# Optimization experiments

Hardware: AMD Instinct MI355X
Metric: run time of the kernel (lower is better)

Reference implementation:

```python
import jax, jax.numpy as jnp
import numpy as np

EMBED_DIM = 2048
NUM_Q_HEADS = 16
NUM_KV_HEADS = 4
HEAD_DIM = EMBED_DIM // NUM_Q_HEADS  # 128
N_REP = NUM_Q_HEADS // NUM_KV_HEADS  # 4


def setup_inputs() -> dict:
    key = jax.random.key(0)
    ks = jax.random.split(key, 8)
    B, T, C = 2, 2048, EMBED_DIM
    s = 0.02
    return {
        "x": jax.random.normal(ks[0], (B, T, C), dtype=jnp.float32),
        "Wq": jax.random.normal(ks[1], (C, NUM_Q_HEADS * HEAD_DIM), dtype=jnp.float32) * s,
        "bq": jax.random.normal(ks[2], (NUM_Q_HEADS * HEAD_DIM,), dtype=jnp.float32) * s,
        "Wk": jax.random.normal(ks[3], (C, NUM_KV_HEADS * HEAD_DIM), dtype=jnp.float32) * s,
        "bk": jax.random.normal(ks[4], (NUM_KV_HEADS * HEAD_DIM,), dtype=jnp.float32) * s,
        "Wv": jax.random.normal(ks[5], (C, NUM_KV_HEADS * HEAD_DIM), dtype=jnp.float32) * s,
        "bv": jax.random.normal(ks[6], (NUM_KV_HEADS * HEAD_DIM,), dtype=jnp.float32) * s,
        "Wo": jax.random.normal(ks[7], (C, C), dtype=jnp.float32) * s,
    }


def reference(x, Wq, bq, Wk, bk, Wv, bv, Wo):
    B, T, C = x.shape
    # Projections (torch Linear with bias; weights stored as [in, out])
    q = (x @ Wq + bq).reshape(B, T, NUM_KV_HEADS, N_REP, HEAD_DIM)
    k = (x @ Wk + bk).reshape(B, T, NUM_KV_HEADS, HEAD_DIM)
    v = (x @ Wv + bv).reshape(B, T, NUM_KV_HEADS, HEAD_DIM)
    # GQA: group query heads per kv head instead of materializing repeated K/V.
    # q: [B, G, n_rep, Tq, d], k/v: [B, G, Tk, d]
    q = q.transpose(0, 2, 3, 1, 4)  # B, G, n_rep, T, d
    k = k.transpose(0, 2, 1, 3)     # B, G, T, d
    v = v.transpose(0, 2, 1, 3)
    scale = 1.0 / jnp.sqrt(jnp.asarray(HEAD_DIM, dtype=x.dtype))
    scores = jnp.einsum('bgnqd,bgkd->bgnqk', q, k) * scale
    attn = jax.nn.softmax(scores, axis=-1)
    out = jnp.einsum('bgnqk,bgkd->bgnqd', attn, v)  # B, G, n_rep, T, d
    # merge heads back: (G, n_rep) -> Hq, then [B, T, C]
    out = out.transpose(0, 3, 1, 2, 4).reshape(B, T, C)
    return out @ Wo
```

## Files before the change

kernel.cpp:

```cpp
#include <hip/hip_runtime.h>
#include <hip/hip_bf16.h>
#include <cstdint>
#include <cstddef>

typedef __bf16 bf16;
typedef __attribute__((ext_vector_type(8))) __bf16 bf16x8;
typedef __attribute__((ext_vector_type(4))) float f32x4;
typedef __attribute__((ext_vector_type(16))) float f32x16;

#define KPAD 136
#define VPAD 72

__device__ __forceinline__ void async16(const void* g, void* l) {
  __builtin_amdgcn_global_load_lds(
      (const __attribute__((address_space(1))) void*)g,
      (__attribute__((address_space(3))) void*)l,
      16, 0, 0);
}

__global__ void cvt_x(const float* __restrict__ in, bf16* __restrict__ out, int n8) {
  int i = blockIdx.x * 256 + threadIdx.x;
  if (i >= n8) return;
  const float* src = in + (size_t)i * 8;
  float4 f0 = *reinterpret_cast<const float4*>(src);
  float4 f1 = *reinterpret_cast<const float4*>(src + 4);
  bf16x8 v = {(bf16)f0.x, (bf16)f0.y, (bf16)f0.z, (bf16)f0.w,
              (bf16)f1.x, (bf16)f1.y, (bf16)f1.z, (bf16)f1.w};
  *reinterpret_cast<bf16x8*>(out + (size_t)i * 8) = v;
}

template <typename CT, bool HAS_BIAS>
__global__ __launch_bounds__(256, 2)
void gemm_bt(const bf16* __restrict__ A, const bf16* __restrict__ Bt,
             const bf16* __restrict__ bias, CT* __restrict__ C,
             int M, int N, int K) {
  __shared__ bf16 smem[4][128 * 64];
  const int tid = threadIdx.x;
  const int wave = tid >> 6, lane = tid & 63;
  const int quad = lane >> 4, l15 = lane & 15;
  const int row0 = blockIdx.y * 128;
  const int col0 = blockIdx.x * 128;
  const int wm = wave & 1, wn = wave >> 1;
  const int sw = l15 & 7;

  const f32x4 fz = {0.f, 0.f, 0.f, 0.f};
  f32x4 acc[4][4];
#pragma unroll
  for (int i = 0; i < 4; ++i)
#pragma unroll
    for (int j = 0; j < 4; ++j) acc[i][j] = fz;

#define STAGE(buf, k0)                                                         \
  {                                                                            \
    _Pragma("unroll")                                                          \
    for (int j = 0; j < 4; ++j) {                                              \
      int c = tid + j * 256;                                                   \
      int r = c >> 3;                                                          \
      int gs = (c & 7) ^ (r & 7);                                              \
      async16(A + (size_t)(row0 + r) * K + (k0) + gs * 8, &smem[(buf)*2][c * 8]);   \
      async16(Bt + (size_t)(col0 + r) * K + (k0) + gs * 8, &smem[(buf)*2 + 1][c * 8]); \
    }                                                                          \
  }

  STAGE(0, 0);
  __syncthreads();

  const int nt = K >> 6;
  for (int t = 0; t < nt; ++t) {
    const int cur = t & 1;
    if (t + 1 < nt) STAGE(cur ^ 1, (t + 1) << 6);

    const bf16* As = smem[cur * 2];
    const bf16* Bs = smem[cur * 2 + 1];
    bf16x8 a[4][2], b[4][2];
#pragma unroll
    for (int mf = 0; mf < 4; ++mf) {
      int ra = wm * 64 + mf * 16 + l15;
      int rb = wn * 64 + mf * 16 + l15;
#pragma unroll
      for (int ks = 0; ks < 2; ++ks) {
        int pg = (ks * 4 + quad) ^ sw;
        a[mf][ks] = *reinterpret_cast<const bf16x8*>(&As[ra * 64 + pg * 8]);
        b[mf][ks] = *reinterpret_cast<const bf16x8*>(&Bs[rb * 64 + pg * 8]);
      }
    }
#pragma unroll
    for (int ks = 0; ks < 2; ++ks)
#pragma unroll
      for (int mf = 0; mf < 4; ++mf)
#pragma unroll
        for (int nf = 0; nf < 4; ++nf)
          acc[mf][nf] = __builtin_amdgcn_mfma_f32_16x16x32_bf16(a[mf][ks], b[nf][ks],
                                                                acc[mf][nf], 0, 0, 0);

    __syncthreads();
  }
#undef STAGE

#pragma unroll
  for (int i = 0; i < 4; ++i) {
    int m = row0 + wm * 64 + i * 16 + quad * 4;
#pragma unroll
    for (int j = 0; j < 4; ++j) {
      int n = col0 + wn * 64 + j * 16 + l15;
      float bv = HAS_BIAS ? (float)bias[n] : 0.f;
#pragma unroll
      for (int r = 0; r < 4; ++r)
        C[(size_t)(m + r) * N + n] = (CT)(acc[i][j][r] + bv);
    }
  }
}

__global__ void transpose2d_cvt(const float* __restrict__ in, bf16* __restrict__ out,
                                int R, int C) {
  __shared__ float t[32][33];
  const int tx = threadIdx.x & 31, ty = threadIdx.x >> 5;
  const int c0 = blockIdx.x * 32, r0 = blockIdx.y * 32;
#pragma unroll
  for (int i = 0; i < 4; ++i)
    t[ty + i * 8][tx] = in[(size_t)(r0 + ty + i * 8) * C + c0 + tx];
  __syncthreads();
#pragma unroll
  for (int i = 0; i < 4; ++i)
    out[(size_t)(c0 + ty + i * 8) * R + r0 + tx] = (bf16)t[tx][ty + i * 8];
}

__global__ void transpose_v(const bf16* __restrict__ QKV, bf16* __restrict__ Vt) {
  const int z = blockIdx.z;
  const int b = z >> 2, g = z & 3;
  const bf16* in = QKV + (size_t)b * 2048 * 3072 + 2560 + g * 128;
  bf16* out = Vt + (size_t)z * 128 * 2048;
  __shared__ bf16 t[32][33];
  const int tx = threadIdx.x & 31, ty = threadIdx.x >> 5;
  const int d0 = blockIdx.x * 32;
  const int t0 = blockIdx.y * 32;
#pragma unroll
  for (int i = 0; i < 4; ++i)
    t[ty + i * 8][tx] = in[(size_t)(t0 + ty + i * 8) * 3072 + d0 + tx];
  __syncthreads();
#pragma unroll
  for (int i = 0; i < 4; ++i)
    out[(size_t)(d0 + ty + i * 8) * 2048 + t0 + tx] = t[tx][ty + i * 8];
}

__global__ void concat_bias(const float* __restrict__ bq, const float* __restrict__ bk,
                            const float* __restrict__ bv, bf16* __restrict__ out) {
  int i = blockIdx.x * 256 + threadIdx.x;
  float v;
  if (i < 2048) v = bq[i];
  else if (i < 2560) v = bk[i - 2048];
  else v = bv[i - 2560];
  out[i] = (bf16)v;
}

__global__ __launch_bounds__(256, 2)
void attn_kernel(const bf16* __restrict__ QKV, const bf16* __restrict__ Vt,
                 bf16* __restrict__ Out) {
  const int bid = blockIdx.x;
  const int qt = bid & 15;
  const int bh = bid >> 4;
  const int b = bh >> 4, h = bh & 15, g = h >> 2;
  const int tid = threadIdx.x;
  const int wave = tid >> 6, lane = tid & 63;
  const int l31 = lane & 31, half = lane >> 5;

  __shared__ bf16 smem[17920];
  bf16* Ks  = smem;
  bf16* Vts = smem + 8704;
  bf16* Qstage = smem;

  const bf16* Qbase = QKV + ((size_t)b * 2048 + qt * 128) * 3072 + h * 128;
#pragma unroll
  for (int j = 0; j < 8; ++j) {
    int c = tid + j * 256;
    *reinterpret_cast<bf16x8*>(&Qstage[(c >> 4) * KPAD + (c & 15) * 8]) =
        *reinterpret_cast<const bf16x8*>(Qbase + (size_t)(c >> 4) * 3072 + (c & 15) * 8);
  }
  __syncthreads();
  bf16x8 qf[8];
#pragma unroll
  for (int ks = 0; ks < 8; ++ks)
    qf[ks] = *reinterpret_cast<const bf16x8*>(
        &Qstage[(wave * 32 + l31) * KPAD + ks * 16 + half * 8]);

  const bf16* Kbase = QKV + (size_t)b * 2048 * 3072 + 2048 + g * 128;
  const bf16* Vbase = Vt + (size_t)(b * 4 + g) * 128 * 2048;

  f32x16 po[4];
#pragma unroll
  for (int j = 0; j < 4; ++j)
#pragma unroll
    for (int r = 0; r < 16; ++r) po[j][r] = 0.f;
  float lsum = 0.f;
  const float sc = 0.08838834764831845f;

  for (int t0 = 0; t0 < 2048; t0 += 64) {
    __syncthreads();
#pragma unroll
    for (int j = 0; j < 4; ++j) {
      int c = tid + j * 256;
      *reinterpret_cast<bf16x8*>(&Ks[(c >> 4) * KPAD + (c & 15) * 8]) =
          *reinterpret_cast<const bf16x8*>(Kbase + (size_t)(t0 + (c >> 4)) * 3072 + (c & 15) * 8);
      *reinterpret_cast<bf16x8*>(&Vts[(c >> 3) * VPAD + (c & 7) * 8]) =
          *reinterpret_cast<const bf16x8*>(Vbase + (size_t)(c >> 3) * 2048 + t0 + (c & 7) * 8);
    }
    __syncthreads();

    f32x16 s[2];
#pragma unroll
    for (int nt = 0; nt < 2; ++nt)
#pragma unroll
      for (int r = 0; r < 16; ++r) s[nt][r] = 0.f;
#pragma unroll
    for (int ks = 0; ks < 8; ++ks) {
#pragma unroll
      for (int nt = 0; nt < 2; ++nt) {
        bf16x8 kf = *reinterpret_cast<const bf16x8*>(
            &Ks[(nt * 32 + l31) * KPAD + ks * 16 + half * 8]);
        s[nt] = __builtin_amdgcn_mfma_f32_32x32x16_bf16(kf, qf[ks], s[nt], 0, 0, 0);
      }
    }

#pragma unroll
    for (int nt = 0; nt < 2; ++nt)
#pragma unroll
      for (int r = 0; r < 16; ++r) {
        float p = __expf(s[nt][r] * sc);
        lsum += p;
        s[nt][r] = p;
      }

#pragma unroll
    for (int ks2 = 0; ks2 < 4; ++ks2) {
      const int nt = ks2 >> 1;
      const int a = (ks2 & 1) * 8;
      uint32_t x0, x1, x2, x3;
      asm("v_cvt_pk_bf16_f32 %0, %1, %2" : "=v"(x0) : "v"(s[nt][a + 0]), "v"(s[nt][a + 1]));
      asm("v_cvt_pk_bf16_f32 %0, %1, %2" : "=v"(x1) : "v"(s[nt][a + 2]), "v"(s[nt][a + 3]));
      asm("v_cvt_pk_bf16_f32 %0, %1, %2" : "=v"(x2) : "v"(s[nt][a + 4]), "v"(s[nt][a + 5]));
      asm("v_cvt_pk_bf16_f32 %0, %1, %2" : "=v"(x3) : "v"(s[nt][a + 6]), "v"(s[nt][a + 7]));
      asm("v_permlane32_swap_b32 %0, %1" : "+v"(x0), "+v"(x2));
      asm("v_permlane32_swap_b32 %0, %1" : "+v"(x1), "+v"(x3));
      union { uint32_t u[4]; bf16x8 v; } pu;
      pu.u[0] = x0; pu.u[1] = x1; pu.u[2] = x2; pu.u[3] = x3;
      const bf16x8 pf = pu.v;
#pragma unroll
      for (int nd = 0; nd < 4; ++nd) {
        bf16x8 vf = *reinterpret_cast<const bf16x8*>(
            &Vts[(nd * 32 + l31) * VPAD + ks2 * 16 + half * 8]);
        po[nd] = __builtin_amdgcn_mfma_f32_32x32x16_bf16(pf, vf, po[nd], 0, 0, 0);
      }
    }
  }

  float l = lsum + __shfl_xor(lsum, 32, 64);
  float inv = 1.0f / l;

  const size_t qrow0 = (size_t)b * 2048 + (size_t)qt * 128 + wave * 32;
#pragma unroll
  for (int r = 0; r < 16; ++r) {
    int row = (r & 3) + 8 * (r >> 2) + 4 * half;
    float invr = __shfl(inv, row, 64);
#pragma unroll
    for (int nt = 0; nt < 4; ++nt)
      Out[(qrow0 + row) * 2048 + h * 128 + nt * 32 + l31] = (bf16)(po[nt][r] * invr);
  }
}

extern "C" void kernel_launch(void* const* d_in, const int* in_sizes, int n_in,
                              void* d_out, int out_size, void* d_ws, size_t ws_size,
                              hipStream_t stream) {
  const float* x  = (const float*)d_in[0];
  const float* Wq = (const float*)d_in[1];
  const float* bq = (const float*)d_in[2];
  const float* Wk = (const float*)d_in[3];
  const float* bk = (const float*)d_in[4];
  const float* Wv = (const float*)d_in[5];
  const float* bv = (const float*)d_in[6];
  const float* Wo = (const float*)d_in[7];
  float* out = (float*)d_out;
  bf16* ws = (bf16*)d_ws;

  bf16* wqkvT = ws;
  bf16* biasq = ws + 6291456;
  bf16* woT   = ws + 6294528;
  bf16* qkv   = ws + 10488832;
  bf16* vt    = ws + 23071744;
  bf16* aout  = ws + 25168896;
  bf16* xb    = ws + 33557504;

  cvt_x<<<4096, 256, 0, stream>>>(x, xb, 1048576);
  transpose2d_cvt<<<dim3(64, 64), 256, 0, stream>>>(Wq, wqkvT, 2048, 2048);
  transpose2d_cvt<<<dim3(16, 64), 256, 0, stream>>>(Wk, wqkvT + 2048 * 2048, 2048, 512);
  transpose2d_cvt<<<dim3(16, 64), 256, 0, stream>>>(Wv, wqkvT + 2560 * 2048, 2048, 512);
  transpose2d_cvt<<<dim3(64, 64), 256, 0, stream>>>(Wo, woT, 2048, 2048);
  concat_bias<<<12, 256, 0, stream>>>(bq, bk, bv, biasq);

  gemm_bt<bf16, true><<<dim3(24, 32), 256, 0, stream>>>(xb, wqkvT, biasq, qkv, 4096, 3072, 2048);

  transpose_v<<<dim3(4, 64, 8), 256, 0, stream>>>(qkv, vt);

  attn_kernel<<<512, 256, 0, stream>>>(qkv, vt, aout);

  gemm_bt<float, false><<<dim3(16, 32), 256, 0, stream>>>(aout, woT, nullptr, out, 4096, 2048, 2048);
}
```

Measured before the change: 296.4 us.

## Double-buffer K/V tiles with async global-to-LDS loads and XOR swizzle

Replaces the synchronous register-staged K/V tile loads in the attention loop with direct global-to-LDS async loads into two buffers, so the next tile is fetched while the current one is computed. The padded LDS layouts are replaced by unpadded XOR-swizzled layouts to avoid bank conflicts, and exp is computed with exp2 and a prescaled constant. LDS use grows to 64KB per block, which may cut occupancy below the two blocks per CU the launch bounds assume. The softmax still has no max subtraction, as before.

New measurement: 300.0 us. No clear change (+1.2%).

```diff
diff --git a/kernel.cpp b/kernel.cpp
--- a/kernel.cpp
+++ b/kernel.cpp
@@ -9,7 +9,6 @@
 typedef __attribute__((ext_vector_type(16))) float f32x16;
 
 #define KPAD 136
-#define VPAD 72
 
 __device__ __forceinline__ void async16(const void* g, void* l) {
   __builtin_amdgcn_global_load_lds(
@@ -164,9 +163,7 @@
   const int wave = tid >> 6, lane = tid & 63;
   const int l31 = lane & 31, half = lane >> 5;
 
-  __shared__ bf16 smem[17920];
-  bf16* Ks  = smem;
-  bf16* Vts = smem + 8704;
+  __shared__ bf16 smem[32768];
   bf16* Qstage = smem;
 
   const bf16* Qbase = QKV + ((size_t)b * 2048 + qt * 128) * 3072 + h * 128;
@@ -182,29 +179,42 @@
   for (int ks = 0; ks < 8; ++ks)
     qf[ks] = *reinterpret_cast<const bf16x8*>(
         &Qstage[(wave * 32 + l31) * KPAD + ks * 16 + half * 8]);
+  __syncthreads();
 
   const bf16* Kbase = QKV + (size_t)b * 2048 * 3072 + 2048 + g * 128;
   const bf16* Vbase = Vt + (size_t)(b * 4 + g) * 128 * 2048;
 
+#define ATTN_STAGE(buf, t0_)                                                  \
+  {                                                                           \
+    bf16* KsD = smem + (buf)*16384;                                           \
+    bf16* VsD = smem + (buf)*16384 + 8192;                                    \
+    _Pragma("unroll")                                                         \
+    for (int j = 0; j < 4; ++j) {                                             \
+      int c = tid + j * 256;                                                  \
+      int rk = c >> 4, gk = (c & 15) ^ (rk & 15);                             \
+      async16(Kbase + (size_t)((t0_) + rk) * 3072 + gk * 8, &KsD[c * 8]);     \
+      int rv = c >> 3, gv = (c & 7) ^ (rv & 7);                               \
+      async16(Vbase + (size_t)rv * 2048 + (t0_) + gv * 8, &VsD[c * 8]);       \
+    }                                                                         \
+  }
+
+  ATTN_STAGE(0, 0);
+  __syncthreads();
+
   f32x16 po[4];
 #pragma unroll
   for (int j = 0; j < 4; ++j)
 #pragma unroll
     for (int r = 0; r < 16; ++r) po[j][r] = 0.f;
   float lsum = 0.f;
-  const float sc = 0.08838834764831845f;
-
-  for (int t0 = 0; t0 < 2048; t0 += 64) {
-    __syncthreads();
-#pragma unroll
-    for (int j = 0; j < 4; ++j) {
-      int c = tid + j * 256;
-      *reinterpret_cast<bf16x8*>(&Ks[(c >> 4) * KPAD + (c & 15) * 8]) =
-          *reinterpret_cast<const bf16x8*>(Kbase + (size_t)(t0 + (c >> 4)) * 3072 + (c & 15) * 8);
-      *reinterpret_cast<bf16x8*>(&Vts[(c >> 3) * VPAD + (c & 7) * 8]) =
-          *reinterpret_cast<const bf16x8*>(Vbase + (size_t)(c >> 3) * 2048 + t0 + (c & 7) * 8);
-    }
-    __syncthreads();
+  const float sc2 = 0.12751746030545063f;
+
+  for (int t = 0; t < 32; ++t) {
+    const int cur = t & 1;
+    if (t + 1 < 32) ATTN_STAGE(cur ^ 1, (t + 1) * 64);
+
+    const bf16* KsB = smem + cur * 16384;
+    const bf16* VsB = smem + cur * 16384 + 8192;
 
     f32x16 s[2];
 #pragma unroll
@@ -216,7 +226,7 @@
 #pragma unroll
       for (int nt = 0; nt < 2; ++nt) {
         bf16x8 kf = *reinterpret_cast<const bf16x8*>(
-            &Ks[(nt * 32 + l31) * KPAD + ks * 16 + half * 8]);
+            &KsB[(nt * 32 + l31) * 128 + (((ks * 2 + half) ^ (l31 & 15))) * 8]);
         s[nt] = __builtin_amdgcn_mfma_f32_32x32x16_bf16(kf, qf[ks], s[nt], 0, 0, 0);
       }
     }
@@ -225,7 +235,7 @@
     for (int nt = 0; nt < 2; ++nt)
 #pragma unroll
       for (int r = 0; r < 16; ++r) {
-        float p = __expf(s[nt][r] * sc);
+        float p = exp2f(s[nt][r] * sc2);
         lsum += p;
         s[nt][r] = p;
       }
@@ -247,11 +257,14 @@
 #pragma unroll
       for (int nd = 0; nd < 4; ++nd) {
         bf16x8 vf = *reinterpret_cast<const bf16x8*>(
-            &Vts[(nd * 32 + l31) * VPAD + ks2 * 16 + half * 8]);
+            &VsB[(nd * 32 + l31) * 64 + (((ks2 * 2 + half) ^ (l31 & 7))) * 8]);
         po[nd] = __builtin_amdgcn_mfma_f32_32x32x16_bf16(pf, vf, po[nd], 0, 0, 0);
       }
     }
-  }
+
+    __syncthreads();
+  }
+#undef ATTN_STAGE
 
   float l = lsum + __shfl_xor(lsum, 32, 64);
   float inv = 1.0f / l;
```
